# Kernel optimization log

Measured on AMD Instinct MI355X. Metric: run time of the kernel, lower is better.

## Reference

```python
import jax, jax.numpy as jnp
import numpy as np
import math

D_MODEL, N_HEADS, BATCH, SEQ = 1024, 16, 2, 2048
D_HEAD = D_MODEL // N_HEADS


def setup_inputs() -> dict:
    key = jax.random.key(0)
    ks = jax.random.split(key, 5)
    w = lambda k: jax.random.normal(k, (D_MODEL, D_MODEL), jnp.float32) * 0.02
    return {
        "X": jax.random.normal(ks[0], (BATCH, SEQ, D_MODEL), jnp.float32),
        "W_q": w(ks[1]),
        "W_k": w(ks[2]),
        "W_v": w(ks[3]),
        "W_o": w(ks[4]),
        "g_q": jnp.ones((D_MODEL,), jnp.float32),
        "b_q": jnp.zeros((D_MODEL,), jnp.float32),
        "g_k": jnp.ones((D_MODEL,), jnp.float32),
        "b_k": jnp.zeros((D_MODEL,), jnp.float32),
        "cache_k": jnp.zeros((BATCH, N_HEADS, SEQ, D_HEAD), jnp.float32),
        "cache_v": jnp.zeros((BATCH, N_HEADS, SEQ, D_HEAD), jnp.float32),
        "start_pos": 0,
    }


def _layernorm(x, g, b, eps=1e-5):
    mu = jnp.mean(x, axis=-1, keepdims=True)
    xc = x - mu
    var = jnp.mean(xc * xc, axis=-1, keepdims=True)
    return xc * jax.lax.rsqrt(var + eps) * g + b


def reference(X, W_q, W_k, W_v, W_o, g_q, b_q, g_k, b_k, cache_k, cache_v, start_pos):
    batch, N, d_model = X.shape
    H = cache_k.shape[1]
    dh = d_model // H

    # QK-normed projections (torch Linear: x @ W^T)
    XQ = _layernorm(X @ W_q.T, g_q, b_q)
    XK = _layernorm(X @ W_k.T, g_k, b_k)
    XV = X @ W_v.T
    split = lambda t: t.reshape(batch, N, H, dh).transpose(0, 2, 1, 3)  # [b,h,n,d]
    XQ, XK, XV = split(XQ), split(XK), split(XV)

    # KV-cache scatter update, then slice to valid prefix (start_pos is static)
    cache_k = jax.lax.dynamic_update_slice(cache_k, XK, (0, 0, start_pos, 0))
    cache_v = jax.lax.dynamic_update_slice(cache_v, XV, (0, 0, start_pos, 0))
    M = start_pos + N
    K = cache_k[:, :, :M]
    V = cache_v[:, :, :M]

    logits = jnp.einsum('bhnd,bhmd->bhnm', XQ, K) / math.sqrt(dh)  # [b,h,N,M]

    # causal mask on the freshly written block [start_pos:M]
    tril = jnp.tril(jnp.ones((N, N), bool))
    full_mask = jnp.concatenate([jnp.ones((N, start_pos), bool), tril], axis=1)  # [N,M]
    logits = jnp.where(full_mask[None, None], logits, -jnp.inf)

    # selective forget-mask bias built from relu'd head-0 logits
    S = jax.nn.relu(logits[:, 0])               # relu(-inf) -> 0, matches torch
    S = S.at[..., 0].set(0.0)                   # zero first column
    S = S * (1.0 - jnp.eye(N, dtype=S.dtype))   # zero diagonal (valid since start_pos==0)
    S = jnp.roll(S, 1, axis=-2)                 # shift rows down by one
    S = S.at[..., 0, :].set(0.0)
    F_mask = jnp.cumsum(S, axis=-2)             # [b,N,M]

    logits = logits - F_mask[:, None]
    attn = jax.nn.softmax(logits, axis=-1)
    O = jnp.einsum('bhnm,bhmd->bhnd', attn, V)
    O = O.transpose(0, 2, 1, 3).reshape(batch, N, d_model)
    return O @ W_o.T
```

## Files before the change

kernel.cpp:

```cpp
#include <hip/hip_runtime.h>
#include <cstdint>
#include <cstddef>


typedef unsigned short u16;
typedef __attribute__((ext_vector_type(8))) __bf16 bf16x8;
typedef __attribute__((ext_vector_type(4))) float f32x4;

#define D_MODEL 1024
#define N_HEADS 16
#define BATCH   2
#define SEQ     2048
#define D_HEAD  64
#define ROWS    (BATCH*SEQ)
#define NSEG    16
#define SEGLEN  128
#define LOG2E   1.44269504f

static __device__ __forceinline__ u16 f2bf(float f){
  union { float f; uint32_t u; } v; v.f = f;
  uint32_t r = v.u + 0x7fffu + ((v.u >> 16) & 1u);
  return (u16)(r >> 16);
}
static __device__ __forceinline__ float bf2f(u16 h){
  union { uint32_t u; float f; } v; v.u = ((uint32_t)h) << 16;
  return v.f;
}
static __device__ __forceinline__ uint32_t pack2(float a, float b){
  uint32_t ua = __float_as_uint(a) + 0x8000u;
  uint32_t ub = __float_as_uint(b) + 0x8000u;
  return (ua >> 16) | (ub & 0xffff0000u);
}

__global__ void k_cast_split_all(const float* __restrict__ X,
                                 u16* __restrict__ Xhi, u16* __restrict__ Xlo,
                                 const float* __restrict__ Wq,
                                 u16* __restrict__ Wqh, u16* __restrict__ Wql,
                                 const float* __restrict__ Wk,
                                 u16* __restrict__ Wkh, u16* __restrict__ Wkl){
  int i = blockIdx.x*256 + threadIdx.x;
  const float* src; u16 *dh, *dl; int base;
  if (i < 1048576){ src = X;  dh = Xhi; dl = Xlo; base = i; }
  else if (i < 1310720){ src = Wq; dh = Wqh; dl = Wql; base = i - 1048576; }
  else { src = Wk; dh = Wkh; dl = Wkl; base = i - 1310720; }
  float4 v = reinterpret_cast<const float4*>(src)[base];
  float vs[4] = {v.x, v.y, v.z, v.w};
  union { u16 s[4]; uint2 u; } uh, ul;
#pragma unroll
  for (int r=0;r<4;++r){
    uh.s[r] = f2bf(vs[r]);
    ul.s[r] = f2bf(vs[r] - bf2f(uh.s[r]));
  }
  reinterpret_cast<uint2*>(dh)[base] = uh.u;
  reinterpret_cast<uint2*>(dl)[base] = ul.u;
}

__global__ void k_cast2(const float* __restrict__ Wv, u16* __restrict__ Wvb,
                        const float* __restrict__ Wo, u16* __restrict__ Wob){
  int i = blockIdx.x*256 + threadIdx.x;
  const float* src; u16* dst; int base;
  if (i < 262144){ src = Wv; dst = Wvb; base = i; }
  else { src = Wo; dst = Wob; base = i - 262144; }
  float4 v = reinterpret_cast<const float4*>(src)[base];
  float vs[4] = {v.x, v.y, v.z, v.w};
  union { u16 s[4]; uint2 u; } uh;
#pragma unroll
  for (int r=0;r<4;++r) uh.s[r] = f2bf(vs[r]);
  reinterpret_cast<uint2*>(dst)[base] = uh.u;
}

__global__ __launch_bounds__(256) void k_gemm_qk(
    const u16* __restrict__ Xhi, const u16* __restrict__ Xlo,
    const u16* __restrict__ Wh, const u16* __restrict__ Wl,
    float* __restrict__ C)
{
  __shared__ __align__(16) u16 As[128*32];
  __shared__ __align__(16) u16 Bs[128*32];
  const int tid = threadIdx.x, wv = tid>>6, ln = tid&63;
  const int lane15 = ln&15, quad = ln>>4;
  const int wm = wv&1, wn = wv>>1;
  const size_t rowBase = (size_t)blockIdx.y*128, colBase = (size_t)blockIdx.x*128;
  const int npass = ((blockIdx.x & 7) == 0) ? 3 : 1;
  f32x4 acc[4][4];
  f32x4 z = {0.f,0.f,0.f,0.f};
#pragma unroll
  for (int i=0;i<4;++i)
#pragma unroll
    for (int j=0;j<4;++j) acc[i][j] = z;
  const u16* Aps[3] = {Xhi, Xhi, Xlo};
  const u16* Bps[3] = {Wh, Wl, Wh};
  const int sRow = ln>>2, sCol = (ln&3)*8;
  for (int p = 0; p < npass; ++p) {
    const u16* Ap = Aps[p];
    const u16* Bp = Bps[p];
    for (int kt = 0; kt < 32; ++kt) {
      __syncthreads();
#pragma unroll
      for (int c = 0; c < 2; ++c) {
        int chunk = wv*2 + c;
        int r = chunk*16 + sRow;
        const u16* ga = Ap + (rowBase + r)*1024 + kt*32 + sCol;
        const u16* gb = Bp + (colBase + r)*1024 + kt*32 + sCol;
        __builtin_amdgcn_global_load_lds(
            (const __attribute__((address_space(1))) void*)ga,
            (__attribute__((address_space(3))) void*)(As + chunk*512), 16, 0, 0);
        __builtin_amdgcn_global_load_lds(
            (const __attribute__((address_space(1))) void*)gb,
            (__attribute__((address_space(3))) void*)(Bs + chunk*512), 16, 0, 0);
      }
      __syncthreads();
      bf16x8 af[4], bfb[4];
#pragma unroll
      for (int t=0;t<4;++t){
        af[t]  = *reinterpret_cast<const bf16x8*>(As + (wm*64 + t*16 + lane15)*32 + quad*8);
        bfb[t] = *reinterpret_cast<const bf16x8*>(Bs + (wn*64 + t*16 + lane15)*32 + quad*8);
      }
#pragma unroll
      for (int i=0;i<4;++i)
#pragma unroll
        for (int j=0;j<4;++j)
          acc[i][j] = __builtin_amdgcn_mfma_f32_16x16x32_bf16(af[i], bfb[j], acc[i][j], 0,0,0);
    }
  }
#pragma unroll
  for (int i=0;i<4;++i){
    size_t row = rowBase + wm*64 + i*16 + quad*4;
#pragma unroll
    for (int j=0;j<4;++j){
      size_t col = colBase + wn*64 + j*16 + lane15;
#pragma unroll
      for (int r=0;r<4;++r)
        C[(row+r)*2048 + col] = acc[i][j][r];
    }
  }
}

__global__ __launch_bounds__(256) void k_ln_pack2(
    const float* __restrict__ C,
    const float* __restrict__ gq, const float* __restrict__ bq,
    const float* __restrict__ gk, const float* __restrict__ bk,
    u16* __restrict__ Qh, u16* __restrict__ Kh,
    u16* __restrict__ Q0l, u16* __restrict__ K0l)
{
  const int row = blockIdx.x;
  const int tid = threadIdx.x;
  const float* cr = C + (size_t)row*2048;
  float4 vq = reinterpret_cast<const float4*>(cr)[tid];
  float4 vk = reinterpret_cast<const float4*>(cr)[256 + tid];
  float sq  = vq.x+vq.y+vq.z+vq.w;
  float s2q = vq.x*vq.x+vq.y*vq.y+vq.z*vq.z+vq.w*vq.w;
  float sk  = vk.x+vk.y+vk.z+vk.w;
  float s2k = vk.x*vk.x+vk.y*vk.y+vk.z*vk.z+vk.w*vk.w;
#pragma unroll
  for (int o=32;o;o>>=1){
    sq += __shfl_xor(sq,o);  s2q += __shfl_xor(s2q,o);
    sk += __shfl_xor(sk,o);  s2k += __shfl_xor(s2k,o);
  }
  __shared__ float red[4][4];
  if ((tid&63)==0){
    red[tid>>6][0]=sq; red[tid>>6][1]=s2q; red[tid>>6][2]=sk; red[tid>>6][3]=s2k;
  }
  __syncthreads();
  sq  = red[0][0]+red[1][0]+red[2][0]+red[3][0];
  s2q = red[0][1]+red[1][1]+red[2][1]+red[3][1];
  sk  = red[0][2]+red[1][2]+red[2][2]+red[3][2];
  s2k = red[0][3]+red[1][3]+red[2][3]+red[3][3];
  const float muq = sq*(1.f/D_MODEL);
  const float rsq = rsqrtf(s2q*(1.f/D_MODEL) - muq*muq + 1e-5f);
  const float muk = sk*(1.f/D_MODEL);
  const float rsk = rsqrtf(s2k*(1.f/D_MODEL) - muk*muk + 1e-5f);
  const int b = row >> 11, n = row & (SEQ-1);
  const int h = tid >> 4, d0 = (tid & 15)*4;
  float4 gqv = reinterpret_cast<const float4*>(gq)[tid];
  float4 bqv = reinterpret_cast<const float4*>(bq)[tid];
  float4 gkv = reinterpret_cast<const float4*>(gk)[tid];
  float4 bkv = reinterpret_cast<const float4*>(bk)[tid];
  float xq[4] = {vq.x,vq.y,vq.z,vq.w}, xk[4] = {vk.x,vk.y,vk.z,vk.w};
  float gQ[4] = {gqv.x,gqv.y,gqv.z,gqv.w}, bQ[4] = {bqv.x,bqv.y,bqv.z,bqv.w};
  float gK[4] = {gkv.x,gkv.y,gkv.z,gkv.w}, bK[4] = {bkv.x,bkv.y,bkv.z,bkv.w};
  union { u16 s[4]; uint2 u; } qh, ql, kh, kl;
#pragma unroll
  for (int r=0;r<4;++r){
    float yq = (xq[r]-muq)*rsq*gQ[r] + bQ[r];
    qh.s[r] = f2bf(yq);
    ql.s[r] = f2bf(yq - bf2f(qh.s[r]));
    float yk = (xk[r]-muk)*rsk*gK[r] + bK[r];
    kh.s[r] = f2bf(yk);
    kl.s[r] = f2bf(yk - bf2f(kh.s[r]));
  }
  size_t dst = (((size_t)(b*N_HEADS + h))*SEQ + n)*D_HEAD + d0;
  *reinterpret_cast<uint2*>(Qh + dst) = qh.u;
  *reinterpret_cast<uint2*>(Kh + dst) = kh.u;
  if (h == 0){
    size_t dl = ((size_t)b*SEQ + n)*D_HEAD + d0;
    *reinterpret_cast<uint2*>(Q0l + dl) = ql.u;
    *reinterpret_cast<uint2*>(K0l + dl) = kl.u;
  }
}

__global__ __launch_bounds__(256) void k_gemm_vt(
    const u16* __restrict__ A0, const u16* __restrict__ B0,
    u16* __restrict__ Vt)
{
  __shared__ __align__(16) u16 smem[64*136];
  u16* As = smem;
  u16* Bs = smem + 128*32;
  const int tid = threadIdx.x, wv = tid>>6, ln = tid&63;
  const int lane15 = ln&15, quad = ln>>4;
  const int wm = wv&1, wn = wv>>1;
  const size_t rowBase = (size_t)blockIdx.y*128, colBase = (size_t)blockIdx.x*64;
  f32x4 acc[4][2];
  f32x4 z = {0.f,0.f,0.f,0.f};
#pragma unroll
  for (int i=0;i<4;++i){ acc[i][0] = z; acc[i][1] = z; }
  const int sRow = ln>>2, sCol = (ln&3)*8;
  for (int kt = 0; kt < 32; ++kt) {
    __syncthreads();
#pragma unroll
    for (int c = 0; c < 2; ++c) {
      int chunk = wv*2 + c;
      int r = chunk*16 + sRow;
      const u16* ga = A0 + (rowBase + r)*1024 + kt*32 + sCol;
      __builtin_amdgcn_global_load_lds(
          (const __attribute__((address_space(1))) void*)ga,
          (__attribute__((address_space(3))) void*)(As + chunk*512), 16, 0, 0);
    }
    {
      int r = wv*16 + sRow;
      const u16* gb = B0 + (colBase + r)*1024 + kt*32 + sCol;
      __builtin_amdgcn_global_load_lds(
          (const __attribute__((address_space(1))) void*)gb,
          (__attribute__((address_space(3))) void*)(Bs + wv*512), 16, 0, 0);
    }
    __syncthreads();
    bf16x8 af[4], bfb[2];
#pragma unroll
    for (int t=0;t<4;++t)
      af[t]  = *reinterpret_cast<const bf16x8*>(As + (wm*64 + t*16 + lane15)*32 + quad*8);
#pragma unroll
    for (int t=0;t<2;++t)
      bfb[t] = *reinterpret_cast<const bf16x8*>(Bs + (wn*32 + t*16 + lane15)*32 + quad*8);
#pragma unroll
    for (int i=0;i<4;++i)
#pragma unroll
      for (int j=0;j<2;++j)
        acc[i][j] = __builtin_amdgcn_mfma_f32_16x16x32_bf16(af[i], bfb[j], acc[i][j], 0,0,0);
  }
  __syncthreads();
#pragma unroll
  for (int i=0;i<4;++i){
    int nl = wm*64 + i*16 + quad*4;
#pragma unroll
    for (int j=0;j<2;++j){
      int dl = wn*32 + j*16 + lane15;
#pragma unroll
      for (int r=0;r<4;++r)
        smem[dl*136 + nl + r] = f2bf(acc[i][j][r]);
    }
  }
  __syncthreads();
  const int b = (int)blockIdx.y >> 4;
  const int n0 = ((int)blockIdx.y & 15) * 128;
  const int bh = b*N_HEADS + (int)blockIdx.x;
  const int d = tid >> 2, seg = tid & 3;
  u16* dst = Vt + ((size_t)(bh*64 + d))*SEQ + n0 + seg*32;
  const u16* srcl = smem + d*136 + seg*32;
#pragma unroll
  for (int k=0;k<4;++k)
    *reinterpret_cast<uint4*>(dst + k*8) = *reinterpret_cast<const uint4*>(srcl + k*8);
}

__global__ __launch_bounds__(256) void k_s0(
    const u16* Qh, const u16* Q0l, const u16* Kh, const u16* K0l,
    float* __restrict__ S0, float* __restrict__ seg)
{
  const int b = blockIdx.z;
  const int bm = blockIdx.y;
  const int bn = blockIdx.x;
  const int tid = threadIdx.x;
  if (bn > bm){
    if (tid < 128) seg[((size_t)b*NSEG + bm)*SEQ + bn*128 + tid] = 0.f;
    return;
  }
  float* Sb = S0 + (size_t)b*SEQ*SEQ;
  __shared__ __align__(16) u16 As[128*32];
  __shared__ __align__(16) u16 Bs[128*32];
  __shared__ float cs[2][128];
  const int wv = tid>>6, ln = tid&63;
  const int lane15 = ln&15, quad = ln>>4;
  const int wm = wv&1, wn = wv>>1;
  f32x4 acc[4][4];
  f32x4 z = {0.f,0.f,0.f,0.f};
#pragma unroll
  for (int i=0;i<4;++i)
#pragma unroll
    for (int j=0;j<4;++j) acc[i][j] = z;
  const u16* Qb  = Qh  + (size_t)b*N_HEADS*SEQ*D_HEAD;
  const u16* Kb  = Kh  + (size_t)b*N_HEADS*SEQ*D_HEAD;
  const u16* Qlb = Q0l + (size_t)b*SEQ*D_HEAD;
  const u16* Klb = K0l + (size_t)b*SEQ*D_HEAD;
  const u16* Aps[3] = {Qb, Qb, Qlb};
  const u16* Bps[3] = {Kb, Klb, Kb};
  const int sRow = ln>>2, sCol = (ln&3)*8;
  const size_t rowBase = (size_t)bm*128, colBase = (size_t)bn*128;
  for (int p = 0; p < 3; ++p) {
    const u16* Ap = Aps[p];
    const u16* Bp = Bps[p];
    for (int kt = 0; kt < 2; ++kt) {
      __syncthreads();
#pragma unroll
      for (int c = 0; c < 2; ++c) {
        int chunk = wv*2 + c;
        int r = chunk*16 + sRow;
        const u16* ga = Ap + (rowBase + r)*D_HEAD + kt*32 + sCol;
        const u16* gb = Bp + (colBase + r)*D_HEAD + kt*32 + sCol;
        __builtin_amdgcn_global_load_lds(
            (const __attribute__((address_space(1))) void*)ga,
            (__attribute__((address_space(3))) void*)(As + chunk*512), 16, 0, 0);
        __builtin_amdgcn_global_load_lds(
            (const __attribute__((address_space(1))) void*)gb,
            (__attribute__((address_space(3))) void*)(Bs + chunk*512), 16, 0, 0);
      }
      __syncthreads();
      bf16x8 af[4], bfb[4];
#pragma unroll
      for (int t=0;t<4;++t){
        af[t]  = *reinterpret_cast<const bf16x8*>(As + (wm*64 + t*16 + lane15)*32 + quad*8);
        bfb[t] = *reinterpret_cast<const bf16x8*>(Bs + (wn*64 + t*16 + lane15)*32 + quad*8);
      }
#pragma unroll
      for (int i=0;i<4;++i)
#pragma unroll
        for (int j=0;j<4;++j)
          acc[i][j] = __builtin_amdgcn_mfma_f32_16x16x32_bf16(af[i], bfb[j], acc[i][j], 0,0,0);
    }
  }
  float csum[4] = {0.f,0.f,0.f,0.f};
#pragma unroll
  for (int i=0;i<4;++i){
#pragma unroll
    for (int j=0;j<4;++j){
#pragma unroll
      for (int r=0;r<4;++r){
        int jg = (int)rowBase + wm*64 + i*16 + quad*4 + r;
        int mg = (int)colBase + wn*64 + j*16 + lane15;
        float l = acc[i][j][r]*0.125f;
        float s = (mg >= 1 && mg < jg) ? fmaxf(l, 0.f) : 0.f;
        Sb[(size_t)jg*SEQ + mg] = s;
        csum[j] += s;
      }
    }
  }
#pragma unroll
  for (int j=0;j<4;++j){
    float v = csum[j];
    v += __shfl_xor(v, 16);
    v += __shfl_xor(v, 32);
    if (ln < 16) cs[wm][wn*64 + j*16 + ln] = v;
  }
  __syncthreads();
  if (tid < 128)
    seg[((size_t)b*NSEG + bm)*SEQ + bn*128 + tid] = cs[0][tid] + cs[1][tid];
}

__global__ void k_seg_scan(float* __restrict__ seg){
  int m = blockIdx.x*256 + threadIdx.x;
  int b = blockIdx.y;
  float run = 0.f;
#pragma unroll
  for (int s=0;s<NSEG;++s){
    size_t idx = ((size_t)b*NSEG + s)*SEQ + m;
    float t = seg[idx]; seg[idx] = run; run += t;
  }
}
__global__ void k_seg_apply(float* __restrict__ SF, const float* __restrict__ seg){
  int m = blockIdx.x*256 + threadIdx.x;
  int s = blockIdx.y, b = blockIdx.z;
  float run = seg[((size_t)b*NSEG + s)*SEQ + m];
  float* Sb = SF + (size_t)b*SEQ*SEQ;
  const int j0 = s*SEGLEN;
  for (int i=0;i<SEGLEN;++i){
    size_t idx = (size_t)(j0 + i)*SEQ + m;
    float t = Sb[idx];
    Sb[idx] = -run*LOG2E;
    run += (j0 + i > m) ? t : 0.f;
  }
}

__global__ __launch_bounds__(256, 4) void k_attn(
    const u16* __restrict__ Qh, const u16* __restrict__ Kh,
    const u16* __restrict__ Vt, const float* __restrict__ F,
    u16* __restrict__ Ob)
{
  __shared__ __align__(16) u16 Ks[2][64*64];
  __shared__ __align__(16) u16 Vs[2][64*64];
  const int h = blockIdx.x, b = blockIdx.z;
  const int nt = b ? (int)(gridDim.y - 1 - blockIdx.y) : (int)blockIdx.y;
  const int tid = threadIdx.x, wv = tid>>6, ln = tid&63;
  const int lane15 = ln&15, quad = ln>>4;
  const u16* Qbh = Qh + ((size_t)(b*N_HEADS + h))*SEQ*D_HEAD;
  const u16* Kbh = Kh + ((size_t)(b*N_HEADS + h))*SEQ*D_HEAD;
  const u16* Vbh = Vt + ((size_t)(b*N_HEADS + h))*D_HEAD*SEQ;
  const float* Fb = F + (size_t)b*SEQ*SEQ;
  const int n_loc = wv*16 + lane15;
  const int n_g = nt*64 + n_loc;
  const int swz = (ln&7) ^ ((ln>>3)&7);
  const int fswz = lane15 & 7;
  const int srow = ln>>3;

  bf16x8 qf[2];
#pragma unroll
  for (int kt=0; kt<2; ++kt)
    qf[kt] = *reinterpret_cast<const bf16x8*>(Qbh + (size_t)n_g*D_HEAD + kt*32 + quad*8);

  f32x4 z = {0.f,0.f,0.f,0.f};
  f32x4 psum = z;
  f32x4 acc_o[4];
#pragma unroll
  for (int no=0;no<4;++no) acc_o[no] = z;

  auto stage = [&](int mt, int buf){
#pragma unroll
    for (int c=0;c<2;++c){
      int chunk = wv*2 + c;
      int r = chunk*8 + srow;
      const u16* gk = Kbh + (size_t)(mt*64 + r)*D_HEAD + swz*8;
      const u16* gv = Vbh + (size_t)r*SEQ + mt*64 + swz*8;
      __builtin_amdgcn_global_load_lds(
          (const __attribute__((address_space(1))) void*)gk,
          (__attribute__((address_space(3))) void*)(&Ks[buf][chunk*512]), 16, 0, 0);
      __builtin_amdgcn_global_load_lds(
          (const __attribute__((address_space(1))) void*)gv,
          (__attribute__((address_space(3))) void*)(&Vs[buf][chunk*512]), 16, 0, 0);
    }
  };
  stage(0, 0);
  const float c1 = 0.125f*LOG2E;

  for (int mt = 0; mt <= nt; ++mt) {
    const int cur = mt & 1;
    __syncthreads();
    if (mt < nt) stage(mt+1, 1-cur);
    const float* Fr = Fb + (size_t)n_g*SEQ + mt*64;
    f32x4 fv[4];
#pragma unroll
    for (int ms=0; ms<4; ++ms)
      fv[ms] = *reinterpret_cast<const f32x4*>(Fr + ms*16 + quad*4);
    f32x4 accs[4];
#pragma unroll
    for (int ms=0;ms<4;++ms) accs[ms] = z;
#pragma unroll
    for (int kt=0; kt<2; ++kt){
#pragma unroll
      for (int ms=0; ms<4; ++ms){
        bf16x8 a = *reinterpret_cast<const bf16x8*>(
            &Ks[cur][(ms*16 + lane15)*64 + (((kt*4 + quad) ^ fswz) * 8)]);
        accs[ms] = __builtin_amdgcn_mfma_f32_16x16x32_bf16(a, qf[kt], accs[ms], 0,0,0);
      }
    }
    const bool diag = (mt == nt);
    uint32_t pw[4][2];
#pragma unroll
    for (int ms=0; ms<4; ++ms){
      f32x4 t = accs[ms];
      float p[4];
#pragma unroll
      for (int r=0;r<4;++r){
        float l2 = fmaf(t[r], c1, fv[ms][r]);
        if (diag){
          int ml = ms*16 + quad*4 + r;
          l2 = (ml > n_loc) ? -1e30f : l2;
        }
        p[r] = __builtin_amdgcn_exp2f(l2);
      }
      psum[0]+=p[0]; psum[1]+=p[1]; psum[2]+=p[2]; psum[3]+=p[3];
      pw[ms][0] = pack2(p[0], p[1]);
      pw[ms][1] = pack2(p[2], p[3]);
    }
#pragma unroll
    for (int kt=0; kt<2; ++kt){
      union { uint32_t u[4]; bf16x8 v; } pa;
#pragma unroll
      for (int w=0; w<4; ++w){
        int sl = lane15 + 16*((quad&1)*2 + (w>>1));
        uint32_t t0 = (uint32_t)__shfl((int)pw[2*kt  ][w&1], sl);
        uint32_t t1 = (uint32_t)__shfl((int)pw[2*kt+1][w&1], sl);
        pa.u[w] = (quad < 2) ? t0 : t1;
      }
#pragma unroll
      for (int no=0; no<4; ++no){
        int d = no*16 + lane15;
        bf16x8 vb = *reinterpret_cast<const bf16x8*>(
            &Vs[cur][d*64 + (((kt*4 + quad) ^ (d&7)) * 8)]);
        acc_o[no] = __builtin_amdgcn_mfma_f32_16x16x32_bf16(pa.v, vb, acc_o[no], 0,0,0);
      }
    }
  }
  float s = (psum[0]+psum[1]) + (psum[2]+psum[3]);
  s += __shfl_xor(s, 16);
  s += __shfl_xor(s, 32);
  f32x4 inv;
#pragma unroll
  for (int r=0;r<4;++r)
    inv[r] = __builtin_amdgcn_rcpf(__shfl(s, quad*4 + r));
#pragma unroll
  for (int no=0; no<4; ++no){
#pragma unroll
    for (int r=0;r<4;++r){
      float o = acc_o[no][r] * inv[r];
      int row = nt*64 + wv*16 + quad*4 + r;
      Ob[((size_t)(b*SEQ + row))*D_MODEL + h*64 + no*16 + lane15] = f2bf(o);
    }
  }
}

__global__ __launch_bounds__(256) void k_gemm_nt64(
    const u16* __restrict__ A0, const u16* __restrict__ B0,
    float* __restrict__ C, int N, int K)
{
  __shared__ __align__(16) u16 As[128*32];
  __shared__ __align__(16) u16 Bs[64*32];
  const int tid = threadIdx.x, wv = tid>>6, ln = tid&63;
  const int lane15 = ln&15, quad = ln>>4;
  const int wm = wv&1, wn = wv>>1;
  const size_t rowBase = (size_t)blockIdx.y*128, colBase = (size_t)blockIdx.x*64;
  f32x4 acc[4][2];
  f32x4 z = {0.f,0.f,0.f,0.f};
#pragma unroll
  for (int i=0;i<4;++i){ acc[i][0] = z; acc[i][1] = z; }
  const int ktiles = K >> 5;
  const int sRow = ln>>2, sCol = (ln&3)*8;
  for (int kt = 0; kt < ktiles; ++kt) {
    __syncthreads();
#pragma unroll
    for (int c = 0; c < 2; ++c) {
      int chunk = wv*2 + c;
      int r = chunk*16 + sRow;
      const u16* ga = A0 + (rowBase + r)*K + kt*32 + sCol;
      __builtin_amdgcn_global_load_lds(
          (const __attribute__((address_space(1))) void*)ga,
          (__attribute__((address_space(3))) void*)(As + chunk*512), 16, 0, 0);
    }
    {
      int r = wv*16 + sRow;
      const u16* gb = B0 + (colBase + r)*K + kt*32 + sCol;
      __builtin_amdgcn_global_load_lds(
          (const __attribute__((address_space(1))) void*)gb,
          (__attribute__((address_space(3))) void*)(Bs + wv*512), 16, 0, 0);
    }
    __syncthreads();
    bf16x8 af[4], bfb[2];
#pragma unroll
    for (int t=0;t<4;++t)
      af[t]  = *reinterpret_cast<const bf16x8*>(As + (wm*64 + t*16 + lane15)*32 + quad*8);
#pragma unroll
    for (int t=0;t<2;++t)
      bfb[t] = *reinterpret_cast<const bf16x8*>(Bs + (wn*32 + t*16 + lane15)*32 + quad*8);
#pragma unroll
    for (int i=0;i<4;++i)
#pragma unroll
      for (int j=0;j<2;++j)
        acc[i][j] = __builtin_amdgcn_mfma_f32_16x16x32_bf16(af[i], bfb[j], acc[i][j], 0,0,0);
  }
#pragma unroll
  for (int i=0;i<4;++i){
    size_t row = rowBase + wm*64 + i*16 + quad*4;
#pragma unroll
    for (int j=0;j<2;++j){
      size_t col = colBase + wn*32 + j*16 + lane15;
#pragma unroll
      for (int r=0;r<4;++r)
        C[(row+r)*N + col] = acc[i][j][r];
    }
  }
}

extern "C" void kernel_launch(void* const* d_in, const int* in_sizes, int n_in,
                              void* d_out, int out_size, void* d_ws, size_t ws_size,
                              hipStream_t stream)
{
  (void)in_sizes; (void)n_in; (void)out_size; (void)ws_size;
  const float* X  = (const float*)d_in[0];
  const float* Wq = (const float*)d_in[1];
  const float* Wk = (const float*)d_in[2];
  const float* Wv = (const float*)d_in[3];
  const float* Wo = (const float*)d_in[4];
  const float* gq = (const float*)d_in[5];
  const float* bq = (const float*)d_in[6];
  const float* gk = (const float*)d_in[7];
  const float* bk = (const float*)d_in[8];
  float* out = (float*)d_out;

  char* ws = (char*)d_ws;
  size_t off = 0;
  auto alloc = [&](size_t bytes)->char*{
    char* p = ws + off; off += (bytes + 255) & ~(size_t)255; return p;
  };
  u16* Xhi  = (u16*)alloc((size_t)ROWS*D_MODEL*2);
  u16* Xlo  = (u16*)alloc((size_t)ROWS*D_MODEL*2);
  u16* Wqkh = (u16*)alloc((size_t)2*D_MODEL*D_MODEL*2);
  u16* Wqkl = (u16*)alloc((size_t)2*D_MODEL*D_MODEL*2);
  u16* Wvb  = (u16*)alloc((size_t)D_MODEL*D_MODEL*2);
  u16* Wob  = (u16*)alloc((size_t)D_MODEL*D_MODEL*2);
  u16* Qhp  = (u16*)alloc((size_t)BATCH*N_HEADS*SEQ*D_HEAD*2);
  u16* Khp  = (u16*)alloc((size_t)BATCH*N_HEADS*SEQ*D_HEAD*2);
  u16* Q0l  = (u16*)alloc((size_t)BATCH*SEQ*D_HEAD*2);
  u16* K0l  = (u16*)alloc((size_t)BATCH*SEQ*D_HEAD*2);
  u16* Vtp  = (u16*)alloc((size_t)BATCH*N_HEADS*D_HEAD*SEQ*2);
  u16* Obf  = (u16*)alloc((size_t)ROWS*D_MODEL*2);
  float* Seg = (float*)alloc((size_t)BATCH*NSEG*SEQ*4);
  float* SF  = (float*)alloc((size_t)BATCH*SEQ*SEQ*4);
  float* C32 = SF;

  k_cast_split_all<<<6144, 256, 0, stream>>>(
      X, Xhi, Xlo,
      Wq, Wqkh, Wqkl,
      Wk, Wqkh + (size_t)D_MODEL*D_MODEL, Wqkl + (size_t)D_MODEL*D_MODEL);
  k_cast2<<<2048, 256, 0, stream>>>(Wv, Wvb, Wo, Wob);

  k_gemm_qk<<<dim3(16, 32), 256, 0, stream>>>(Xhi, Xlo, Wqkh, Wqkl, C32);
  k_ln_pack2<<<ROWS, 256, 0, stream>>>(C32, gq, bq, gk, bk, Qhp, Khp, Q0l, K0l);
  k_gemm_vt<<<dim3(16, 32), 256, 0, stream>>>(Xhi, Wvb, Vtp);
  k_s0<<<dim3(16, 16, BATCH), 256, 0, stream>>>(Qhp, Q0l, Khp, K0l, SF, Seg);
  k_seg_scan<<<dim3(8, BATCH), 256, 0, stream>>>(Seg);
  k_seg_apply<<<dim3(8, NSEG, BATCH), 256, 0, stream>>>(SF, Seg);
  k_attn<<<dim3(N_HEADS, SEQ/64, BATCH), 256, 0, stream>>>(Qhp, Khp, Vtp, SF, Obf);
  k_gemm_nt64<<<dim3(16, 32), 256, 0, stream>>>(Obf, Wob, out, D_MODEL, D_MODEL);
}
```

Baseline: 331.4 us.

## Split QK correction GEMM out, fold seg scan, and widen attention tiles

The QK projection GEMM previously ran three passes in the head-0 column blocks and one pass elsewhere, which left those blocks imbalanced. That work is now split into a uniform single-pass GEMM plus a separate small correction GEMM. Its output is added during layernorm. The separate segment-scan kernel is removed; each seg_apply block now recomputes its prefix sum directly. The attention kernel processes 128 query rows per block instead of 64, so each staged K/V tile is reused across two row groups. The cost is more registers and fewer blocks in flight.

```diff
diff --git a/kernel.cpp b/kernel.cpp
--- a/kernel.cpp
+++ b/kernel.cpp
@@ -61,17 +61,17 @@
   const float* src; u16* dst; int base;
   if (i < 262144){ src = Wv; dst = Wvb; base = i; }
   else { src = Wo; dst = Wob; base = i - 262144; }
-  float4 v = reinterpret_cast<const float4*>(src)[base];
+  float4 v = reinterpret_cast<const float4*>(src)[i < 262144 ? i : i - 262144];
+  (void)base;
   float vs[4] = {v.x, v.y, v.z, v.w};
   union { u16 s[4]; uint2 u; } uh;
 #pragma unroll
   for (int r=0;r<4;++r) uh.s[r] = f2bf(vs[r]);
-  reinterpret_cast<uint2*>(dst)[base] = uh.u;
+  reinterpret_cast<uint2*>(dst)[i < 262144 ? i : i - 262144] = uh.u;
 }
 
 __global__ __launch_bounds__(256) void k_gemm_qk(
-    const u16* __restrict__ Xhi, const u16* __restrict__ Xlo,
-    const u16* __restrict__ Wh, const u16* __restrict__ Wl,
+    const u16* __restrict__ A0, const u16* __restrict__ B0,
     float* __restrict__ C)
 {
   __shared__ __align__(16) u16 As[128*32];
@@ -80,17 +80,74 @@
   const int lane15 = ln&15, quad = ln>>4;
   const int wm = wv&1, wn = wv>>1;
   const size_t rowBase = (size_t)blockIdx.y*128, colBase = (size_t)blockIdx.x*128;
-  const int npass = ((blockIdx.x & 7) == 0) ? 3 : 1;
   f32x4 acc[4][4];
   f32x4 z = {0.f,0.f,0.f,0.f};
 #pragma unroll
   for (int i=0;i<4;++i)
 #pragma unroll
     for (int j=0;j<4;++j) acc[i][j] = z;
-  const u16* Aps[3] = {Xhi, Xhi, Xlo};
-  const u16* Bps[3] = {Wh, Wl, Wh};
   const int sRow = ln>>2, sCol = (ln&3)*8;
-  for (int p = 0; p < npass; ++p) {
+  for (int kt = 0; kt < 32; ++kt) {
+    __syncthreads();
+#pragma unroll
+    for (int c = 0; c < 2; ++c) {
+      int chunk = wv*2 + c;
+      int r = chunk*16 + sRow;
+      const u16* ga = A0 + (rowBase + r)*1024 + kt*32 + sCol;
+      const u16* gb = B0 + (colBase + r)*1024 + kt*32 + sCol;
+      __builtin_amdgcn_global_load_lds(
+          (const __attribute__((address_space(1))) void*)ga,
+          (__attribute__((address_space(3))) void*)(As + chunk*512), 16, 0, 0);
+      __builtin_amdgcn_global_load_lds(
+          (const __attribute__((address_space(1))) void*)gb,
+          (__attribute__((address_space(3))) void*)(Bs + chunk*512), 16, 0, 0);
+    }
+    __syncthreads();
+    bf16x8 af[4], bfb[4];
+#pragma unroll
+    for (int t=0;t<4;++t){
+      af[t]  = *reinterpret_cast<const bf16x8*>(As + (wm*64 + t*16 + lane15)*32 + quad*8);
+      bfb[t] = *reinterpret_cast<const bf16x8*>(Bs + (wn*64 + t*16 + lane15)*32 + quad*8);
+    }
+#pragma unroll
+    for (int i=0;i<4;++i)
+#pragma unroll
+      for (int j=0;j<4;++j)
+        acc[i][j] = __builtin_amdgcn_mfma_f32_16x16x32_bf16(af[i], bfb[j], acc[i][j], 0,0,0);
+  }
+#pragma unroll
+  for (int i=0;i<4;++i){
+    size_t row = rowBase + wm*64 + i*16 + quad*4;
+#pragma unroll
+    for (int j=0;j<4;++j){
+      size_t col = colBase + wn*64 + j*16 + lane15;
+#pragma unroll
+      for (int r=0;r<4;++r)
+        C[(row+r)*2048 + col] = acc[i][j][r];
+    }
+  }
+}
+
+__global__ __launch_bounds__(256) void k_gemm_corr(
+    const u16* __restrict__ Xhi, const u16* __restrict__ Xlo,
+    const u16* __restrict__ Wh, const u16* __restrict__ Wl,
+    float* __restrict__ Dlt)
+{
+  __shared__ __align__(16) u16 As[128*32];
+  __shared__ __align__(16) u16 Bs[64*32];
+  const int tid = threadIdx.x, wv = tid>>6, ln = tid&63;
+  const int lane15 = ln&15, quad = ln>>4;
+  const int wm = wv&1, wn = wv>>1;
+  const size_t rowBase = (size_t)blockIdx.y*128;
+  const size_t wrow0 = blockIdx.x ? 1024 : 0;
+  f32x4 acc[4][2];
+  f32x4 z = {0.f,0.f,0.f,0.f};
+#pragma unroll
+  for (int i=0;i<4;++i){ acc[i][0] = z; acc[i][1] = z; }
+  const int sRow = ln>>2, sCol = (ln&3)*8;
+  const u16* Aps[2] = {Xhi, Xlo};
+  const u16* Bps[2] = {Wl + wrow0*1024, Wh + wrow0*1024};
+  for (int p = 0; p < 2; ++p){
     const u16* Ap = Aps[p];
     const u16* Bp = Bps[p];
     for (int kt = 0; kt < 32; ++kt) {
@@ -100,25 +157,29 @@
         int chunk = wv*2 + c;
         int r = chunk*16 + sRow;
         const u16* ga = Ap + (rowBase + r)*1024 + kt*32 + sCol;
-        const u16* gb = Bp + (colBase + r)*1024 + kt*32 + sCol;
         __builtin_amdgcn_global_load_lds(
             (const __attribute__((address_space(1))) void*)ga,
             (__attribute__((address_space(3))) void*)(As + chunk*512), 16, 0, 0);
+      }
+      {
+        int r = wv*16 + sRow;
+        const u16* gb = Bp + (size_t)r*1024 + kt*32 + sCol;
         __builtin_amdgcn_global_load_lds(
             (const __attribute__((address_space(1))) void*)gb,
-            (__attribute__((address_space(3))) void*)(Bs + chunk*512), 16, 0, 0);
+            (__attribute__((address_space(3))) void*)(Bs + wv*512), 16, 0, 0);
       }
       __syncthreads();
-      bf16x8 af[4], bfb[4];
-#pragma unroll
-      for (int t=0;t<4;++t){
+      bf16x8 af[4], bfb[2];
+#pragma unroll
+      for (int t=0;t<4;++t)
         af[t]  = *reinterpret_cast<const bf16x8*>(As + (wm*64 + t*16 + lane15)*32 + quad*8);
-        bfb[t] = *reinterpret_cast<const bf16x8*>(Bs + (wn*64 + t*16 + lane15)*32 + quad*8);
-      }
+#pragma unroll
+      for (int t=0;t<2;++t)
+        bfb[t] = *reinterpret_cast<const bf16x8*>(Bs + (wn*32 + t*16 + lane15)*32 + quad*8);
 #pragma unroll
       for (int i=0;i<4;++i)
 #pragma unroll
-        for (int j=0;j<4;++j)
+        for (int j=0;j<2;++j)
           acc[i][j] = __builtin_amdgcn_mfma_f32_16x16x32_bf16(af[i], bfb[j], acc[i][j], 0,0,0);
     }
   }
@@ -126,17 +187,17 @@
   for (int i=0;i<4;++i){
     size_t row = rowBase + wm*64 + i*16 + quad*4;
 #pragma unroll
-    for (int j=0;j<4;++j){
-      size_t col = colBase + wn*64 + j*16 + lane15;
+    for (int j=0;j<2;++j){
+      size_t col = (size_t)blockIdx.x*64 + wn*32 + j*16 + lane15;
 #pragma unroll
       for (int r=0;r<4;++r)
-        C[(row+r)*2048 + col] = acc[i][j][r];
+        Dlt[(row+r)*128 + col] = acc[i][j][r];
     }
   }
 }
 
 __global__ __launch_bounds__(256) void k_ln_pack2(
-    const float* __restrict__ C,
+    const float* __restrict__ C, const float* __restrict__ Dlt,
     const float* __restrict__ gq, const float* __restrict__ bq,
     const float* __restrict__ gk, const float* __restrict__ bk,
     u16* __restrict__ Qh, u16* __restrict__ Kh,
@@ -176,6 +237,12 @@
   float4 gkv = reinterpret_cast<const float4*>(gk)[tid];
   float4 bkv = reinterpret_cast<const float4*>(bk)[tid];
   float xq[4] = {vq.x,vq.y,vq.z,vq.w}, xk[4] = {vk.x,vk.y,vk.z,vk.w};
+  if (h == 0){
+    float4 dq = reinterpret_cast<const float4*>(Dlt + (size_t)row*128)[tid&15];
+    float4 dk = reinterpret_cast<const float4*>(Dlt + (size_t)row*128 + 64)[tid&15];
+    xq[0]+=dq.x; xq[1]+=dq.y; xq[2]+=dq.z; xq[3]+=dq.w;
+    xk[0]+=dk.x; xk[1]+=dk.y; xk[2]+=dk.z; xk[3]+=dk.w;
+  }
   float gQ[4] = {gqv.x,gqv.y,gqv.z,gqv.w}, bQ[4] = {bqv.x,bqv.y,bqv.z,bqv.w};
   float gK[4] = {gkv.x,gkv.y,gkv.z,gkv.w}, bK[4] = {bkv.x,bkv.y,bkv.z,bkv.w};
   union { u16 s[4]; uint2 u; } qh, ql, kh, kl;
@@ -363,20 +430,12 @@
     seg[((size_t)b*NSEG + bm)*SEQ + bn*128 + tid] = cs[0][tid] + cs[1][tid];
 }
 
-__global__ void k_seg_scan(float* __restrict__ seg){
-  int m = blockIdx.x*256 + threadIdx.x;
-  int b = blockIdx.y;
-  float run = 0.f;
-#pragma unroll
-  for (int s=0;s<NSEG;++s){
-    size_t idx = ((size_t)b*NSEG + s)*SEQ + m;
-    float t = seg[idx]; seg[idx] = run; run += t;
-  }
-}
 __global__ void k_seg_apply(float* __restrict__ SF, const float* __restrict__ seg){
   int m = blockIdx.x*256 + threadIdx.x;
   int s = blockIdx.y, b = blockIdx.z;
-  float run = seg[((size_t)b*NSEG + s)*SEQ + m];
+  const float* sb = seg + (size_t)b*NSEG*SEQ;
+  float run = 0.f;
+  for (int t=0; t<s; ++t) run += sb[(size_t)t*SEQ + m];
   float* Sb = SF + (size_t)b*SEQ*SEQ;
   const int j0 = s*SEGLEN;
   for (int i=0;i<SEGLEN;++i){
@@ -402,30 +461,36 @@
   const u16* Kbh = Kh + ((size_t)(b*N_HEADS + h))*SEQ*D_HEAD;
   const u16* Vbh = Vt + ((size_t)(b*N_HEADS + h))*D_HEAD*SEQ;
   const float* Fb = F + (size_t)b*SEQ*SEQ;
-  const int n_loc = wv*16 + lane15;
-  const int n_g = nt*64 + n_loc;
+  const int n0 = nt*128;
   const int swz = (ln&7) ^ ((ln>>3)&7);
   const int fswz = lane15 & 7;
   const int srow = ln>>3;
-
-  bf16x8 qf[2];
-#pragma unroll
-  for (int kt=0; kt<2; ++kt)
-    qf[kt] = *reinterpret_cast<const bf16x8*>(Qbh + (size_t)n_g*D_HEAD + kt*32 + quad*8);
+  const int nchunks = 2*nt + 2;
+
+  bf16x8 qf[2][2];
+#pragma unroll
+  for (int ns=0; ns<2; ++ns)
+#pragma unroll
+    for (int kt=0; kt<2; ++kt){
+      int n = n0 + wv*32 + ns*16 + lane15;
+      qf[ns][kt] = *reinterpret_cast<const bf16x8*>(Qbh + (size_t)n*D_HEAD + kt*32 + quad*8);
+    }
 
   f32x4 z = {0.f,0.f,0.f,0.f};
-  f32x4 psum = z;
-  f32x4 acc_o[4];
-#pragma unroll
-  for (int no=0;no<4;++no) acc_o[no] = z;
-
-  auto stage = [&](int mt, int buf){
+  f32x4 psum[2] = {z, z};
+  f32x4 acc_o[2][4];
+#pragma unroll
+  for (int ns=0;ns<2;++ns)
+#pragma unroll
+    for (int no=0;no<4;++no) acc_o[ns][no] = z;
+
+  auto stage = [&](int mc, int buf){
 #pragma unroll
     for (int c=0;c<2;++c){
       int chunk = wv*2 + c;
       int r = chunk*8 + srow;
-      const u16* gk = Kbh + (size_t)(mt*64 + r)*D_HEAD + swz*8;
-      const u16* gv = Vbh + (size_t)r*SEQ + mt*64 + swz*8;
+      const u16* gk = Kbh + (size_t)(mc*64 + r)*D_HEAD + swz*8;
+      const u16* gv = Vbh + (size_t)r*SEQ + mc*64 + swz*8;
       __builtin_amdgcn_global_load_lds(
           (const __attribute__((address_space(1))) void*)gk,
           (__attribute__((address_space(3))) void*)(&Ks[buf][chunk*512]), 16, 0, 0);
@@ -437,79 +502,87 @@
   stage(0, 0);
   const float c1 = 0.125f*LOG2E;
 
-  for (int mt = 0; mt <= nt; ++mt) {
-    const int cur = mt & 1;
+  for (int mc = 0; mc < nchunks; ++mc) {
+    const int cur = mc & 1;
     __syncthreads();
-    if (mt < nt) stage(mt+1, 1-cur);
-    const float* Fr = Fb + (size_t)n_g*SEQ + mt*64;
-    f32x4 fv[4];
-#pragma unroll
-    for (int ms=0; ms<4; ++ms)
-      fv[ms] = *reinterpret_cast<const f32x4*>(Fr + ms*16 + quad*4);
-    f32x4 accs[4];
-#pragma unroll
-    for (int ms=0;ms<4;++ms) accs[ms] = z;
-#pragma unroll
-    for (int kt=0; kt<2; ++kt){
+    if (mc+1 < nchunks) stage(mc+1, 1-cur);
+    const bool diag = (mc >= 2*nt);
+#pragma unroll
+    for (int ns=0; ns<2; ++ns){
+      const int n_loc = wv*32 + ns*16 + lane15;
+      const int n_g = n0 + n_loc;
+      const float* Fr = Fb + (size_t)n_g*SEQ + mc*64;
+      f32x4 fv[4];
+#pragma unroll
+      for (int ms=0; ms<4; ++ms)
+        fv[ms] = *reinterpret_cast<const f32x4*>(Fr + ms*16 + quad*4);
+      f32x4 accs[4];
+#pragma unroll
+      for (int ms=0;ms<4;++ms) accs[ms] = z;
+#pragma unroll
+      for (int kt=0; kt<2; ++kt){
+#pragma unroll
+        for (int ms=0; ms<4; ++ms){
+          bf16x8 a = *reinterpret_cast<const bf16x8*>(
+              &Ks[cur][(ms*16 + lane15)*64 + (((kt*4 + quad) ^ fswz) * 8)]);
+          accs[ms] = __builtin_amdgcn_mfma_f32_16x16x32_bf16(a, qf[ns][kt], accs[ms], 0,0,0);
+        }
+      }
+      uint32_t pw[4][2];
 #pragma unroll
       for (int ms=0; ms<4; ++ms){
-        bf16x8 a = *reinterpret_cast<const bf16x8*>(
-            &Ks[cur][(ms*16 + lane15)*64 + (((kt*4 + quad) ^ fswz) * 8)]);
-        accs[ms] = __builtin_amdgcn_mfma_f32_16x16x32_bf16(a, qf[kt], accs[ms], 0,0,0);
-      }
-    }
-    const bool diag = (mt == nt);
-    uint32_t pw[4][2];
-#pragma unroll
-    for (int ms=0; ms<4; ++ms){
-      f32x4 t = accs[ms];
-      float p[4];
+        f32x4 t = accs[ms];
+        float p[4];
+#pragma unroll
+        for (int r=0;r<4;++r){
+          float l2 = fmaf(t[r], c1, fv[ms][r]);
+          if (diag){
+            int m_g = mc*64 + ms*16 + quad*4 + r;
+            l2 = (m_g > n_g) ? -1e30f : l2;
+          }
+          p[r] = __builtin_amdgcn_exp2f(l2);
+        }
+        psum[ns][0]+=p[0]; psum[ns][1]+=p[1]; psum[ns][2]+=p[2]; psum[ns][3]+=p[3];
+        pw[ms][0] = pack2(p[0], p[1]);
+        pw[ms][1] = pack2(p[2], p[3]);
+      }
+#pragma unroll
+      for (int kt=0; kt<2; ++kt){
+        union { uint32_t u[4]; bf16x8 v; } pa;
+#pragma unroll
+        for (int w=0; w<4; ++w){
+          int sl = lane15 + 16*((quad&1)*2 + (w>>1));
+          uint32_t t0 = (uint32_t)__shfl((int)pw[2*kt  ][w&1], sl);
+          uint32_t t1 = (uint32_t)__shfl((int)pw[2*kt+1][w&1], sl);
+          pa.u[w] = (quad < 2) ? t0 : t1;
+        }
+#pragma unroll
+        for (int no=0; no<4; ++no){
+          int d = no*16 + lane15;
+          bf16x8 vb = *reinterpret_cast<const bf16x8*>(
+              &Vs[cur][d*64 + (((kt*4 + quad) ^ (d&7)) * 8)]);
+          acc_o[ns][no] = __builtin_amdgcn_mfma_f32_16x16x32_bf16(pa.v, vb, acc_o[ns][no], 0,0,0);
+        }
+      }
+    }
+  }
+#pragma unroll
+  for (int ns=0; ns<2; ++ns){
+    float s = (psum[ns][0]+psum[ns][1]) + (psum[ns][2]+psum[ns][3]);
+    s += __shfl_xor(s, 16);
+    s += __shfl_xor(s, 32);
+    f32x4 inv;
+#pragma unroll
+    for (int r=0;r<4;++r)
+      inv[r] = __builtin_amdgcn_rcpf(__shfl(s, quad*4 + r));
+#pragma unroll
+    for (int no=0; no<4; ++no){
 #pragma unroll
       for (int r=0;r<4;++r){
-        float l2 = fmaf(t[r], c1, fv[ms][r]);
-        if (diag){
-          int ml = ms*16 + quad*4 + r;
-          l2 = (ml > n_loc) ? -1e30f : l2;
-        }
-        p[r] = __builtin_amdgcn_exp2f(l2);
-      }
-      psum[0]+=p[0]; psum[1]+=p[1]; psum[2]+=p[2]; psum[3]+=p[3];
-      pw[ms][0] = pack2(p[0], p[1]);
-      pw[ms][1] = pack2(p[2], p[3]);
-    }
-#pragma unroll
-    for (int kt=0; kt<2; ++kt){
-      union { uint32_t u[4]; bf16x8 v; } pa;
-#pragma unroll
-      for (int w=0; w<4; ++w){
-        int sl = lane15 + 16*((quad&1)*2 + (w>>1));
-        uint32_t t0 = (uint32_t)__shfl((int)pw[2*kt  ][w&1], sl);
-        uint32_t t1 = (uint32_t)__shfl((int)pw[2*kt+1][w&1], sl);
-        pa.u[w] = (quad < 2) ? t0 : t1;
-      }
-#pragma unroll
-      for (int no=0; no<4; ++no){
-        int d = no*16 + lane15;
-        bf16x8 vb = *reinterpret_cast<const bf16x8*>(
-            &Vs[cur][d*64 + (((kt*4 + quad) ^ (d&7)) * 8)]);
-        acc_o[no] = __builtin_amdgcn_mfma_f32_16x16x32_bf16(pa.v, vb, acc_o[no], 0,0,0);
-      }
-    }
-  }
-  float s = (psum[0]+psum[1]) + (psum[2]+psum[3]);
-  s += __shfl_xor(s, 16);
-  s += __shfl_xor(s, 32);
-  f32x4 inv;
-#pragma unroll
-  for (int r=0;r<4;++r)
-    inv[r] = __builtin_amdgcn_rcpf(__shfl(s, quad*4 + r));
-#pragma unroll
-  for (int no=0; no<4; ++no){
-#pragma unroll
-    for (int r=0;r<4;++r){
-      float o = acc_o[no][r] * inv[r];
-      int row = nt*64 + wv*16 + quad*4 + r;
-      Ob[((size_t)(b*SEQ + row))*D_MODEL + h*64 + no*16 + lane15] = f2bf(o);
+        float o = acc_o[ns][no][r] * inv[r];
+        int row = n0 + wv*32 + ns*16 + quad*4 + r;
+        Ob[((size_t)(b*SEQ + row))*D_MODEL + h*64 + no*16 + lane15] = f2bf(o);
+      }
     }
   }
 }
@@ -608,6 +681,7 @@
   u16* K0l  = (u16*)alloc((size_t)BATCH*SEQ*D_HEAD*2);
   u16* Vtp  = (u16*)alloc((size_t)BATCH*N_HEADS*D_HEAD*SEQ*2);
   u16* Obf  = (u16*)alloc((size_t)ROWS*D_MODEL*2);
+  float* Dlt = (float*)alloc((size_t)ROWS*128*4);
   float* Seg = (float*)alloc((size_t)BATCH*NSEG*SEQ*4);
   float* SF  = (float*)alloc((size_t)BATCH*SEQ*SEQ*4);
   float* C32 = SF;
@@ -618,12 +692,12 @@
       Wk, Wqkh + (size_t)D_MODEL*D_MODEL, Wqkl + (size_t)D_MODEL*D_MODEL);
   k_cast2<<<2048, 256, 0, stream>>>(Wv, Wvb, Wo, Wob);
 
-  k_gemm_qk<<<dim3(16, 32), 256, 0, stream>>>(Xhi, Xlo, Wqkh, Wqkl, C32);
-  k_ln_pack2<<<ROWS, 256, 0, stream>>>(C32, gq, bq, gk, bk, Qhp, Khp, Q0l, K0l);
+  k_gemm_qk<<<dim3(16, 32), 256, 0, stream>>>(Xhi, Wqkh, C32);
+  k_gemm_corr<<<dim3(2, 32), 256, 0, stream>>>(Xhi, Xlo, Wqkh, Wqkl, Dlt);
+  k_ln_pack2<<<ROWS, 256, 0, stream>>>(C32, Dlt, gq, bq, gk, bk, Qhp, Khp, Q0l, K0l);
   k_gemm_vt<<<dim3(16, 32), 256, 0, stream>>>(Xhi, Wvb, Vtp);
   k_s0<<<dim3(16, 16, BATCH), 256, 0, stream>>>(Qhp, Q0l, Khp, K0l, SF, Seg);
-  k_seg_scan<<<dim3(8, BATCH), 256, 0, stream>>>(Seg);
   k_seg_apply<<<dim3(8, NSEG, BATCH), 256, 0, stream>>>(SF, Seg);
-  k_attn<<<dim3(N_HEADS, SEQ/64, BATCH), 256, 0, stream>>>(Qhp, Khp, Vtp, SF, Obf);
+  k_attn<<<dim3(N_HEADS, SEQ/128, BATCH), 256, 0, stream>>>(Qhp, Khp, Vtp, SF, Obf);
   k_gemm_nt64<<<dim3(16, 32), 256, 0, stream>>>(Obf, Wob, out, D_MODEL, D_MODEL);
 }
```

Result: slower. 418.5 us (+26.3%).
